# Performance work log

Measured on AMD Instinct MI355X. Metric: run time of the kernel, lower is better.

Reference implementation:

```python
import jax, jax.numpy as jnp
import numpy as np

NH = 8      # num_heads
NP_ = 4     # num_points

def setup_inputs() -> dict:
    key = jax.random.key(0)
    ks = jax.random.split(key, 12)
    B, N, C = 8, 4096, 256
    query = jax.random.normal(ks[0], (B, N, C), jnp.float32)
    value = jax.random.normal(ks[1], (B, N, C), jnp.float32)
    reference_points = jax.random.uniform(ks[2], (B, N, 2), jnp.float32)
    xav = lambda k, i, o: jax.random.normal(k, (i, o), jnp.float32) * np.sqrt(2.0 / (i + o)).astype(np.float32)
    W_off = jax.random.normal(ks[3], (C, NH * NP_ * 2), jnp.float32) * 0.02  # small offsets (orig inits to 0)
    b_off = jax.random.normal(ks[4], (NH * NP_ * 2,), jnp.float32) * 0.02
    W_attn = xav(ks[5], C, NH * NP_)
    b_attn = jnp.zeros((NH * NP_,), jnp.float32)
    W_val = xav(ks[6], C, C)
    b_val = jnp.zeros((C,), jnp.float32)
    W_out = xav(ks[7], C, C)
    b_out = jnp.zeros((C,), jnp.float32)
    return dict(query=query, value=value, reference_points=reference_points,
                W_off=W_off, b_off=b_off, W_attn=W_attn, b_attn=b_attn,
                W_val=W_val, b_val=b_val, W_out=W_out, b_out=b_out)

def _deform_attn(query, value, reference_points, W_off, b_off, W_attn, b_attn, W_val, b_val, W_out, b_out):
    B, N, C = query.shape
    HW = value.shape[1]
    H = W = int(np.sqrt(HW))  # static
    hd = C // NH
    # value projection -> [B, NH, H*W, hd]
    vals = (value @ W_val + b_val).reshape(B, H, W, NH, hd)
    vals = vals.transpose(0, 3, 1, 2, 4).reshape(B, NH, H * W, hd)
    # offsets [B,N,NH,P,2] in [-0.5,0.5]; attention weights softmax over P
    off = jnp.tanh((query @ W_off + b_off).reshape(B, N, NH, NP_, 2)) * 0.5
    attn = jax.nn.softmax((query @ W_attn + b_attn).reshape(B, N, NH, NP_), axis=-1)
    # sampling locations in [0,1], then grid coords in [-1,1] (x=width, y=height)
    loc = jnp.clip(reference_points[:, :, None, None, :] + off, 0.0, 1.0)
    g = loc * 2.0 - 1.0
    # torch grid_sample, align_corners=False: pixel = (g+1)*size/2 - 0.5
    x = (g[..., 0] + 1.0) * (W * 0.5) - 0.5
    y = (g[..., 1] + 1.0) * (H * 0.5) - 0.5
    x0f = jnp.floor(x); y0f = jnp.floor(y)
    wx1 = x - x0f; wx0 = 1.0 - wx1
    wy1 = y - y0f; wy0 = 1.0 - wy1
    x0 = x0f.astype(jnp.int32); x1 = x0 + 1
    y0 = y0f.astype(jnp.int32); y1 = y0 + 1

    def corner(xi, yi, w):  # xi,yi,w: [B,N,NH,P]; zero padding outside
        valid = (xi >= 0) & (xi < W) & (yi >= 0) & (yi < H)
        idx = jnp.clip(yi, 0, H - 1) * W + jnp.clip(xi, 0, W - 1)
        idx_h = idx.transpose(0, 2, 1, 3).reshape(B, NH, N * NP_)      # [B,NH,N*P]
        gat = jnp.take_along_axis(vals, idx_h[..., None], axis=2)      # [B,NH,N*P,hd]
        wv = jnp.where(valid, w, 0.0).transpose(0, 2, 1, 3).reshape(B, NH, N * NP_)
        return gat * wv[..., None]

    sampled = (corner(x0, y0, wx0 * wy0) + corner(x1, y0, wx1 * wy0)
               + corner(x0, y1, wx0 * wy1) + corner(x1, y1, wx1 * wy1))
    sampled = sampled.reshape(B, NH, N, NP_, hd)
    attn_h = attn.transpose(0, 2, 1, 3)                                 # [B,NH,N,P]
    out = jnp.einsum('bhnpd,bhnp->bnhd', sampled, attn_h).reshape(B, N, C)
    return out @ W_out + b_out  # dropout is identity in eval

def reference(query, value, reference_points, W_off, b_off, W_attn, b_attn, W_val, b_val, W_out, b_out):
    return _deform_attn(query, value, reference_points, W_off, b_off, W_attn, b_attn, W_val, b_val, W_out, b_out)
```

## Files before the change

### kernel.cpp

```cpp
#include <hip/hip_runtime.h>
#include <math.h>

#define NHEAD 8
#define NPT 4
#define HDIM 32
#define IMG 64
#define CDIM 256
#define NQ 4096
#define BATCH 8
#define MTOT (BATCH * NQ)

typedef __attribute__((ext_vector_type(8))) short bf16x8;
typedef __attribute__((ext_vector_type(4))) float f32x4;

__device__ __forceinline__ unsigned short f2b(float f) {
    union { float f; unsigned u; } v; v.f = f;
    unsigned r = (v.u + 0x7FFFu + ((v.u >> 16) & 1u)) >> 16;
    return (unsigned short)r;
}
__device__ __forceinline__ float b2f(unsigned short u) {
    union { unsigned u; float f; } v; v.u = ((unsigned)u) << 16;
    return v.f;
}

#define SWZ(row, col) ((col) ^ (((row) & 7) << 3))


__global__ __launch_bounds__(256)
void cvt_weights_kernel(const float* __restrict__ Wv, const float* __restrict__ Wo,
                        const float* __restrict__ Woff, const float* __restrict__ Wattn,
                        const float* __restrict__ boff, const float* __restrict__ battn,
                        unsigned short* __restrict__ Wv_t, unsigned short* __restrict__ Wo_t,
                        unsigned short* __restrict__ Wl_h, unsigned short* __restrict__ Wl_l,
                        float* __restrict__ bias_lin)
{
    int tid = blockIdx.x * 256 + threadIdx.x;
    int n = tid & 255, k = tid >> 8;
    Wv_t[n * 256 + k] = f2b(Wv[k * 256 + n]);
    Wo_t[n * 256 + k] = f2b(Wo[k * 256 + n]);
    if (tid < 128 * 256) {
        int nn = tid >> 8;
        int kk = tid & 255;
        float v = (nn < 64) ? Woff[kk * 64 + nn]
                : (nn < 96) ? Wattn[kk * 32 + (nn - 64)] : 0.f;
        unsigned short hi = f2b(v);
        unsigned short lo = f2b(v - b2f(hi));
        Wl_h[nn * 256 + kk] = hi;
        Wl_l[nn * 256 + kk] = lo;
    }
    if (tid < 128)
        bias_lin[tid] = (tid < 64) ? boff[tid] : (tid < 96) ? battn[tid - 64] : 0.f;
}

__global__ __launch_bounds__(256)
void lin_gemm_kernel(const float* __restrict__ Q,
                     const unsigned short* __restrict__ Wl_h,
                     const unsigned short* __restrict__ Wl_l,
                     const float* __restrict__ bias,
                     float* __restrict__ lin)
{
    __shared__ unsigned short Ah[128][64], Al[128][64];
    __shared__ unsigned short Bh[128][64], Bl[128][64];

    const int tid  = threadIdx.x;
    const int lane = tid & 63;
    const int wid  = tid >> 6;
    const int gm = ((blockIdx.x & 7) << 12) + ((blockIdx.x >> 3) << 7);
    const int wr = (wid >> 1) * 64;
    const int wc = (wid & 1) * 64;
    const int l15 = lane & 15;
    const int lk  = (lane >> 4) * 8;

    f32x4 acc[4][4];
    #pragma unroll
    for (int m = 0; m < 4; ++m)
        #pragma unroll
        for (int n = 0; n < 4; ++n)
            #pragma unroll
            for (int r = 0; r < 4; ++r) acc[m][n][r] = 0.f;

    for (int k0 = 0; k0 < 256; k0 += 64) {
        #pragma unroll
        for (int it = 0; it < 4; ++it) {
            const int chunk = it * 256 + tid;
            const int row = chunk >> 3;
            const int kc  = (chunk & 7) << 3;
            const float4* src = (const float4*)&Q[(size_t)(gm + row) * 256 + k0 + kc];
            const float4 a = src[0], b = src[1];
            float f[8] = {a.x, a.y, a.z, a.w, b.x, b.y, b.z, b.w};
            unsigned short h[8], l[8];
            #pragma unroll
            for (int j = 0; j < 8; ++j) {
                h[j] = f2b(f[j]);
                l[j] = f2b(f[j] - b2f(h[j]));
            }
            const int sc = SWZ(row, kc);
            *(uint4*)&Ah[row][sc] = *(const uint4*)h;
            *(uint4*)&Al[row][sc] = *(const uint4*)l;
            *(uint4*)&Bh[row][sc] = *(const uint4*)&Wl_h[(size_t)row * 256 + k0 + kc];
            *(uint4*)&Bl[row][sc] = *(const uint4*)&Wl_l[(size_t)row * 256 + k0 + kc];
        }
        __syncthreads();

        #pragma unroll
        for (int kk = 0; kk < 64; kk += 32) {
            bf16x8 ah[4], al[4];
            #pragma unroll
            for (int m = 0; m < 4; ++m) {
                const int r = wr + m * 16 + l15;
                const int c = SWZ(r, kk + lk);
                ah[m] = *(const bf16x8*)&Ah[r][c];
                al[m] = *(const bf16x8*)&Al[r][c];
            }
            if (wc == 0) {
                bf16x8 bh[4], bl[4];
                #pragma unroll
                for (int n = 0; n < 4; ++n) {
                    const int r = n * 16 + l15;
                    const int c = SWZ(r, kk + lk);
                    bh[n] = *(const bf16x8*)&Bh[r][c];
                    bl[n] = *(const bf16x8*)&Bl[r][c];
                }
                #pragma unroll
                for (int m = 0; m < 4; ++m)
                    #pragma unroll
                    for (int n = 0; n < 4; ++n) {
                        acc[m][n] = __builtin_amdgcn_mfma_f32_16x16x32_bf16(ah[m], bh[n], acc[m][n], 0, 0, 0);
                        acc[m][n] = __builtin_amdgcn_mfma_f32_16x16x32_bf16(ah[m], bl[n], acc[m][n], 0, 0, 0);
                        acc[m][n] = __builtin_amdgcn_mfma_f32_16x16x32_bf16(al[m], bh[n], acc[m][n], 0, 0, 0);
                    }
            } else {
                bf16x8 bh[2], bl[2];
                #pragma unroll
                for (int n = 0; n < 2; ++n) {
                    const int r = 64 + n * 16 + l15;
                    const int c = SWZ(r, kk + lk);
                    bh[n] = *(const bf16x8*)&Bh[r][c];
                    bl[n] = *(const bf16x8*)&Bl[r][c];
                }
                #pragma unroll
                for (int m = 0; m < 4; ++m)
                    #pragma unroll
                    for (int n = 0; n < 2; ++n) {
                        acc[m][n] = __builtin_amdgcn_mfma_f32_16x16x32_bf16(ah[m], bh[n], acc[m][n], 0, 0, 0);
                        acc[m][n] = __builtin_amdgcn_mfma_f32_16x16x32_bf16(ah[m], bl[n], acc[m][n], 0, 0, 0);
                        acc[m][n] = __builtin_amdgcn_mfma_f32_16x16x32_bf16(al[m], bh[n], acc[m][n], 0, 0, 0);
                    }
            }
        }
        __syncthreads();
    }

    const int cr = (lane >> 4) * 4;
    #pragma unroll
    for (int n = 0; n < 4; ++n) {
        const int col = wc + n * 16 + l15;
        if (col < 96) {
            const float bv = bias[col];
            #pragma unroll
            for (int m = 0; m < 4; ++m)
                #pragma unroll
                for (int r = 0; r < 4; ++r) {
                    const int row = gm + wr + m * 16 + cr + r;
                    lin[(size_t)row * 96 + col] = acc[m][n][r] + bv;
                }
        }
    }
}

template<bool A_F32, bool OUT_BF16>
__global__ __launch_bounds__(256)
void gemm_bf16_kernel(const void* __restrict__ Ap,
                      const unsigned short* __restrict__ Bt,
                      const float* __restrict__ bias,
                      void* __restrict__ C)
{
    __shared__ unsigned short As[128][64];
    __shared__ unsigned short Bs[128][64];

    const int tid  = threadIdx.x;
    const int lane = tid & 63;
    const int wid  = tid >> 6;
    const int gm = ((blockIdx.x & 7) << 12) + ((blockIdx.x >> 3) << 7);
    const int gn = blockIdx.y * 128;
    const int wr = (wid >> 1) * 64;
    const int wc = (wid & 1) * 64;
    const int l15 = lane & 15;
    const int lk  = (lane >> 4) * 8;

    f32x4 acc[4][4];
    #pragma unroll
    for (int m = 0; m < 4; ++m)
        #pragma unroll
        for (int n = 0; n < 4; ++n)
            #pragma unroll
            for (int r = 0; r < 4; ++r) acc[m][n][r] = 0.f;

    for (int k0 = 0; k0 < 256; k0 += 64) {
        #pragma unroll
        for (int it = 0; it < 4; ++it) {
            const int chunk = it * 256 + tid;
            const int row = chunk >> 3;
            const int kc  = (chunk & 7) << 3;
            const int sc = SWZ(row, kc);
            if (A_F32) {
                const float4* src = (const float4*)&((const float*)Ap)[(size_t)(gm + row) * 256 + k0 + kc];
                const float4 a = src[0], b = src[1];
                float f[8] = {a.x, a.y, a.z, a.w, b.x, b.y, b.z, b.w};
                unsigned short h[8];
                #pragma unroll
                for (int j = 0; j < 8; ++j) h[j] = f2b(f[j]);
                *(uint4*)&As[row][sc] = *(const uint4*)h;
            } else {
                *(uint4*)&As[row][sc] =
                    *(const uint4*)&((const unsigned short*)Ap)[(size_t)(gm + row) * 256 + k0 + kc];
            }
            *(uint4*)&Bs[row][sc] = *(const uint4*)&Bt[(size_t)(gn + row) * 256 + k0 + kc];
        }
        __syncthreads();

        #pragma unroll
        for (int kk = 0; kk < 64; kk += 32) {
            bf16x8 a[4], b[4];
            #pragma unroll
            for (int m = 0; m < 4; ++m) {
                const int r = wr + m * 16 + l15;
                a[m] = *(const bf16x8*)&As[r][SWZ(r, kk + lk)];
            }
            #pragma unroll
            for (int n = 0; n < 4; ++n) {
                const int r = wc + n * 16 + l15;
                b[n] = *(const bf16x8*)&Bs[r][SWZ(r, kk + lk)];
            }
            #pragma unroll
            for (int m = 0; m < 4; ++m)
                #pragma unroll
                for (int n = 0; n < 4; ++n)
                    acc[m][n] = __builtin_amdgcn_mfma_f32_16x16x32_bf16(a[m], b[n], acc[m][n], 0, 0, 0);
        }
        __syncthreads();
    }

    const int cr = (lane >> 4) * 4;
    #pragma unroll
    for (int n = 0; n < 4; ++n) {
        const int col = gn + wc + n * 16 + l15;
        const float bv = bias[col];
        #pragma unroll
        for (int m = 0; m < 4; ++m) {
            #pragma unroll
            for (int r = 0; r < 4; ++r) {
                const int row = gm + wr + m * 16 + cr + r;
                const float v = acc[m][n][r] + bv;
                if (OUT_BF16)
                    ((unsigned short*)C)[(size_t)row * 256 + col] = f2b(v);
                else
                    ((float*)C)[(size_t)row * 256 + col] = v;
            }
        }
    }
}

__global__ __launch_bounds__(256)
void sample_gather_kernel(const unsigned short* __restrict__ projv,
                          const float* __restrict__ lin,
                          const float* __restrict__ refp,
                          unsigned short* __restrict__ sampled)
{
    __shared__ float4 s_w[4][32];
    __shared__ unsigned s_xy[4][32];

    const int i = blockIdx.x;
    const int b = i & 7;
    const int bn0 = (b << 12) + ((i >> 3) << 2);
    const int t = threadIdx.x;

    if (t < 128) {
        const int sub = t >> 5;
        const int q = t & 31;
        const int h = q >> 2;
        const int p = q & 3;
        const int bn = bn0 + sub;
        const float2 rp = *(const float2*)&refp[(size_t)bn * 2];
        const float2 ol = *(const float2*)&lin[(size_t)bn * 96 + h * 8 + p * 2];
        const float al  = lin[(size_t)bn * 96 + 64 + q];

        float mx = al;
        mx = fmaxf(mx, __shfl_xor(mx, 1));
        mx = fmaxf(mx, __shfl_xor(mx, 2));
        float e = expf(al - mx);
        float s = e;
        s += __shfl_xor(s, 1);
        s += __shfl_xor(s, 2);
        const float aw = e / s;

        const float lx = fminf(fmaxf(rp.x + tanhf(ol.x) * 0.5f, 0.f), 1.f);
        const float ly = fminf(fmaxf(rp.y + tanhf(ol.y) * 0.5f, 0.f), 1.f);
        const float x = lx * (float)IMG - 0.5f;
        const float y = ly * (float)IMG - 0.5f;
        const float x0f = floorf(x), y0f = floorf(y);
        const int x0 = (int)x0f, y0 = (int)y0f;
        const float wx1 = x - x0f, wx0 = 1.f - wx1;
        const float wy1 = y - y0f, wy0 = 1.f - wy1;
        const bool vx0 = (x0 >= 0), vx1 = (x0 + 1 < IMG);
        const bool vy0 = (y0 >= 0), vy1 = (y0 + 1 < IMG);
        float4 w;
        w.x = (vx0 && vy0) ? wx0 * wy0 * aw : 0.f;
        w.y = (vx1 && vy0) ? wx1 * wy0 * aw : 0.f;
        w.z = (vx0 && vy1) ? wx0 * wy1 * aw : 0.f;
        w.w = (vx1 && vy1) ? wx1 * wy1 * aw : 0.f;
        const int x0c = min(max(x0, 0), IMG - 1), x1c = min(max(x0 + 1, 0), IMG - 1);
        const int y0c = min(max(y0, 0), IMG - 1), y1c = min(max(y0 + 1, 0), IMG - 1);
        s_w[sub][q] = w;
        s_xy[sub][q] = (unsigned)x0c | ((unsigned)x1c << 8) | ((unsigned)y0c << 16) | ((unsigned)y1c << 24);
    }
    __syncthreads();

    const int sub = t >> 6;
    const int l = t & 63;
    const int h2 = l >> 3;
    const int cp = l & 7;
    const int bn = bn0 + sub;
    const unsigned short* vbase = projv + ((size_t)b << 20) + h2 * HDIM + cp * 4;

    float a0 = 0.f, a1 = 0.f, a2 = 0.f, a3 = 0.f;
    #pragma unroll
    for (int p = 0; p < 4; ++p) {
        const float4 w = s_w[sub][h2 * 4 + p];
        const unsigned xy = s_xy[sub][h2 * 4 + p];
        const int x0 = xy & 255, x1 = (xy >> 8) & 255;
        const int y0 = (xy >> 16) & 255, y1 = xy >> 24;
        const uint2 u00 = *(const uint2*)&vbase[(((y0 << 6) + x0) << 8)];
        const uint2 u01 = *(const uint2*)&vbase[(((y0 << 6) + x1) << 8)];
        const uint2 u10 = *(const uint2*)&vbase[(((y1 << 6) + x0) << 8)];
        const uint2 u11 = *(const uint2*)&vbase[(((y1 << 6) + x1) << 8)];
        a0 += w.x * b2f((unsigned short)(u00.x & 0xffff)) + w.y * b2f((unsigned short)(u01.x & 0xffff))
            + w.z * b2f((unsigned short)(u10.x & 0xffff)) + w.w * b2f((unsigned short)(u11.x & 0xffff));
        a1 += w.x * b2f((unsigned short)(u00.x >> 16)) + w.y * b2f((unsigned short)(u01.x >> 16))
            + w.z * b2f((unsigned short)(u10.x >> 16)) + w.w * b2f((unsigned short)(u11.x >> 16));
        a2 += w.x * b2f((unsigned short)(u00.y & 0xffff)) + w.y * b2f((unsigned short)(u01.y & 0xffff))
            + w.z * b2f((unsigned short)(u10.y & 0xffff)) + w.w * b2f((unsigned short)(u11.y & 0xffff));
        a3 += w.x * b2f((unsigned short)(u00.y >> 16)) + w.y * b2f((unsigned short)(u01.y >> 16))
            + w.z * b2f((unsigned short)(u10.y >> 16)) + w.w * b2f((unsigned short)(u11.y >> 16));
    }
    uint2 outp;
    outp.x = (unsigned)f2b(a0) | ((unsigned)f2b(a1) << 16);
    outp.y = (unsigned)f2b(a2) | ((unsigned)f2b(a3) << 16);
    *(uint2*)&sampled[(size_t)bn * 256 + h2 * HDIM + cp * 4] = outp;
}

extern "C" void kernel_launch(void* const* d_in, const int* in_sizes, int n_in,
                              void* d_out, int out_size, void* d_ws, size_t ws_size,
                              hipStream_t stream)
{
    const float* query  = (const float*)d_in[0];
    const float* value  = (const float*)d_in[1];
    const float* refp   = (const float*)d_in[2];
    const float* W_off  = (const float*)d_in[3];
    const float* b_off  = (const float*)d_in[4];
    const float* W_attn = (const float*)d_in[5];
    const float* b_attn = (const float*)d_in[6];
    const float* W_val  = (const float*)d_in[7];
    const float* b_val  = (const float*)d_in[8];
    const float* W_out  = (const float*)d_in[9];
    const float* b_out  = (const float*)d_in[10];
    float* out = (float*)d_out;

    char* ws = (char*)d_ws;
    unsigned short* projv    = (unsigned short*)ws; ws += (size_t)MTOT * 256 * 2;
    unsigned short* sampled  = (unsigned short*)ws; ws += (size_t)MTOT * 256 * 2;
    float*          lin      = (float*)ws;          ws += (size_t)MTOT * 96 * 4;
    unsigned short* Wv_t     = (unsigned short*)ws; ws += 256 * 256 * 2;
    unsigned short* Wo_t     = (unsigned short*)ws; ws += 256 * 256 * 2;
    unsigned short* Wl_h     = (unsigned short*)ws; ws += 128 * 256 * 2;
    unsigned short* Wl_l     = (unsigned short*)ws; ws += 128 * 256 * 2;
    float*          bias_lin = (float*)ws;          ws += 128 * 4;

    dim3 blk(256);

    cvt_weights_kernel<<<dim3(256), blk, 0, stream>>>(W_val, W_out, W_off, W_attn, b_off, b_attn,
                                                      Wv_t, Wo_t, Wl_h, Wl_l, bias_lin);

    gemm_bf16_kernel<true, true><<<dim3(MTOT / 128, 2), blk, 0, stream>>>(value, Wv_t, b_val, projv);

    lin_gemm_kernel<<<dim3(MTOT / 128), blk, 0, stream>>>(query, Wl_h, Wl_l, bias_lin, lin);

    sample_gather_kernel<<<dim3(MTOT / 4), blk, 0, stream>>>(projv, lin, refp, sampled);

    gemm_bf16_kernel<false, false><<<dim3(MTOT / 128, 2), blk, 0, stream>>>(sampled, Wo_t, b_out, out);
}
```

Baseline: 72.04 us.

## Use direct global-to-LDS loads for bf16 GEMM tiles and double queries per gather block

Weight and bf16 activation tiles in the GEMM kernels are now loaded with global_load_lds (direct-to-LDS, 16 bytes per lane), with the XOR swizzle applied on the global source column, so the data no longer passes through registers. The sampling kernel now handles 8 queries per block in two passes, with all 256 threads computing sampling metadata, which halves the grid size. The goal is to cut register traffic and instruction count in the tile loads and to amortize block setup in the gather. In exchange it depends on direct-to-LDS layout semantics being correct and gives the gather kernel less block-level parallelism.

```diff
diff --git a/kernel.cpp b/kernel.cpp
--- a/kernel.cpp
+++ b/kernel.cpp
@@ -24,6 +24,12 @@
 }
 
 #define SWZ(row, col) ((col) ^ (((row) & 7) << 3))
+
+__device__ __forceinline__ void gload16(const void* src, void* ldsbase) {
+    __builtin_amdgcn_global_load_lds(
+        (const __attribute__((address_space(1))) void*)src,
+        (__attribute__((address_space(3))) void*)ldsbase, 16, 0, 0);
+}
 
 
 __global__ __launch_bounds__(256)
@@ -70,6 +76,8 @@
     const int wc = (wid & 1) * 64;
     const int l15 = lane & 15;
     const int lk  = (lane >> 4) * 8;
+    const int rl  = lane >> 3;
+    const int ch  = (lane & 7) ^ (rl & 7);
 
     f32x4 acc[4][4];
     #pragma unroll
@@ -80,6 +88,12 @@
             for (int r = 0; r < 4; ++r) acc[m][n][r] = 0.f;
 
     for (int k0 = 0; k0 < 256; k0 += 64) {
+        #pragma unroll
+        for (int it = 0; it < 4; ++it) {
+            const int br = it * 32 + wid * 8;
+            gload16(&Wl_h[(size_t)(br + rl) * 256 + k0 + ch * 8], &Bh[br][0]);
+            gload16(&Wl_l[(size_t)(br + rl) * 256 + k0 + ch * 8], &Bl[br][0]);
+        }
         #pragma unroll
         for (int it = 0; it < 4; ++it) {
             const int chunk = it * 256 + tid;
@@ -97,8 +111,6 @@
             const int sc = SWZ(row, kc);
             *(uint4*)&Ah[row][sc] = *(const uint4*)h;
             *(uint4*)&Al[row][sc] = *(const uint4*)l;
-            *(uint4*)&Bh[row][sc] = *(const uint4*)&Wl_h[(size_t)row * 256 + k0 + kc];
-            *(uint4*)&Bl[row][sc] = *(const uint4*)&Wl_l[(size_t)row * 256 + k0 + kc];
         }
         __syncthreads();
 
@@ -187,6 +199,8 @@
     const int wc = (wid & 1) * 64;
     const int l15 = lane & 15;
     const int lk  = (lane >> 4) * 8;
+    const int rl  = lane >> 3;
+    const int ch  = (lane & 7) ^ (rl & 7);
 
     f32x4 acc[4][4];
     #pragma unroll
@@ -199,23 +213,29 @@
     for (int k0 = 0; k0 < 256; k0 += 64) {
         #pragma unroll
         for (int it = 0; it < 4; ++it) {
-            const int chunk = it * 256 + tid;
-            const int row = chunk >> 3;
-            const int kc  = (chunk & 7) << 3;
-            const int sc = SWZ(row, kc);
-            if (A_F32) {
+            const int br = it * 32 + wid * 8;
+            gload16(&Bt[(size_t)(gn + br + rl) * 256 + k0 + ch * 8], &Bs[br][0]);
+        }
+        if (A_F32) {
+            #pragma unroll
+            for (int it = 0; it < 4; ++it) {
+                const int chunk = it * 256 + tid;
+                const int row = chunk >> 3;
+                const int kc  = (chunk & 7) << 3;
                 const float4* src = (const float4*)&((const float*)Ap)[(size_t)(gm + row) * 256 + k0 + kc];
                 const float4 a = src[0], b = src[1];
                 float f[8] = {a.x, a.y, a.z, a.w, b.x, b.y, b.z, b.w};
                 unsigned short h[8];
                 #pragma unroll
                 for (int j = 0; j < 8; ++j) h[j] = f2b(f[j]);
-                *(uint4*)&As[row][sc] = *(const uint4*)h;
-            } else {
-                *(uint4*)&As[row][sc] =
-                    *(const uint4*)&((const unsigned short*)Ap)[(size_t)(gm + row) * 256 + k0 + kc];
-            }
-            *(uint4*)&Bs[row][sc] = *(const uint4*)&Bt[(size_t)(gn + row) * 256 + k0 + kc];
+                *(uint4*)&As[row][SWZ(row, kc)] = *(const uint4*)h;
+            }
+        } else {
+            #pragma unroll
+            for (int it = 0; it < 4; ++it) {
+                const int br = it * 32 + wid * 8;
+                gload16(&((const unsigned short*)Ap)[(size_t)(gm + br + rl) * 256 + k0 + ch * 8], &As[br][0]);
+            }
         }
         __syncthreads();
 
@@ -267,15 +287,15 @@
                           const float* __restrict__ refp,
                           unsigned short* __restrict__ sampled)
 {
-    __shared__ float4 s_w[4][32];
-    __shared__ unsigned s_xy[4][32];
+    __shared__ float4 s_w[8][32];
+    __shared__ unsigned s_xy[8][32];
 
     const int i = blockIdx.x;
     const int b = i & 7;
-    const int bn0 = (b << 12) + ((i >> 3) << 2);
+    const int bn0 = (b << 12) + ((i >> 3) << 3);
     const int t = threadIdx.x;
 
-    if (t < 128) {
+    {
         const int sub = t >> 5;
         const int q = t & 31;
         const int h = q >> 2;
@@ -316,37 +336,41 @@
     }
     __syncthreads();
 
-    const int sub = t >> 6;
     const int l = t & 63;
     const int h2 = l >> 3;
     const int cp = l & 7;
-    const int bn = bn0 + sub;
     const unsigned short* vbase = projv + ((size_t)b << 20) + h2 * HDIM + cp * 4;
 
-    float a0 = 0.f, a1 = 0.f, a2 = 0.f, a3 = 0.f;
     #pragma unroll
-    for (int p = 0; p < 4; ++p) {
-        const float4 w = s_w[sub][h2 * 4 + p];
-        const unsigned xy = s_xy[sub][h2 * 4 + p];
-        const int x0 = xy & 255, x1 = (xy >> 8) & 255;
-        const int y0 = (xy >> 16) & 255, y1 = xy >> 24;
-        const uint2 u00 = *(const uint2*)&vbase[(((y0 << 6) + x0) << 8)];
-        const uint2 u01 = *(const uint2*)&vbase[(((y0 << 6) + x1) << 8)];
-        const uint2 u10 = *(const uint2*)&vbase[(((y1 << 6) + x0) << 8)];
-        const uint2 u11 = *(const uint2*)&vbase[(((y1 << 6) + x1) << 8)];
-        a0 += w.x * b2f((unsigned short)(u00.x & 0xffff)) + w.y * b2f((unsigned short)(u01.x & 0xffff))
-            + w.z * b2f((unsigned short)(u10.x & 0xffff)) + w.w * b2f((unsigned short)(u11.x & 0xffff));
-        a1 += w.x * b2f((unsigned short)(u00.x >> 16)) + w.y * b2f((unsigned short)(u01.x >> 16))
-            + w.z * b2f((unsigned short)(u10.x >> 16)) + w.w * b2f((unsigned short)(u11.x >> 16));
-        a2 += w.x * b2f((unsigned short)(u00.y & 0xffff)) + w.y * b2f((unsigned short)(u01.y & 0xffff))
-            + w.z * b2f((unsigned short)(u10.y & 0xffff)) + w.w * b2f((unsigned short)(u11.y & 0xffff));
-        a3 += w.x * b2f((unsigned short)(u00.y >> 16)) + w.y * b2f((unsigned short)(u01.y >> 16))
-            + w.z * b2f((unsigned short)(u10.y >> 16)) + w.w * b2f((unsigned short)(u11.y >> 16));
-    }
-    uint2 outp;
-    outp.x = (unsigned)f2b(a0) | ((unsigned)f2b(a1) << 16);
-    outp.y = (unsigned)f2b(a2) | ((unsigned)f2b(a3) << 16);
-    *(uint2*)&sampled[(size_t)bn * 256 + h2 * HDIM + cp * 4] = outp;
+    for (int pass = 0; pass < 2; ++pass) {
+        const int sub = (t >> 6) + pass * 4;
+        const int bn = bn0 + sub;
+
+        float a0 = 0.f, a1 = 0.f, a2 = 0.f, a3 = 0.f;
+        #pragma unroll
+        for (int p = 0; p < 4; ++p) {
+            const float4 w = s_w[sub][h2 * 4 + p];
+            const unsigned xy = s_xy[sub][h2 * 4 + p];
+            const int x0 = xy & 255, x1 = (xy >> 8) & 255;
+            const int y0 = (xy >> 16) & 255, y1 = xy >> 24;
+            const uint2 u00 = *(const uint2*)&vbase[(((y0 << 6) + x0) << 8)];
+            const uint2 u01 = *(const uint2*)&vbase[(((y0 << 6) + x1) << 8)];
+            const uint2 u10 = *(const uint2*)&vbase[(((y1 << 6) + x0) << 8)];
+            const uint2 u11 = *(const uint2*)&vbase[(((y1 << 6) + x1) << 8)];
+            a0 += w.x * b2f((unsigned short)(u00.x & 0xffff)) + w.y * b2f((unsigned short)(u01.x & 0xffff))
+                + w.z * b2f((unsigned short)(u10.x & 0xffff)) + w.w * b2f((unsigned short)(u11.x & 0xffff));
+            a1 += w.x * b2f((unsigned short)(u00.x >> 16)) + w.y * b2f((unsigned short)(u01.x >> 16))
+                + w.z * b2f((unsigned short)(u10.x >> 16)) + w.w * b2f((unsigned short)(u11.x >> 16));
+            a2 += w.x * b2f((unsigned short)(u00.y & 0xffff)) + w.y * b2f((unsigned short)(u01.y & 0xffff))
+                + w.z * b2f((unsigned short)(u10.y & 0xffff)) + w.w * b2f((unsigned short)(u11.y & 0xffff));
+            a3 += w.x * b2f((unsigned short)(u00.y >> 16)) + w.y * b2f((unsigned short)(u01.y >> 16))
+                + w.z * b2f((unsigned short)(u10.y >> 16)) + w.w * b2f((unsigned short)(u11.y >> 16));
+        }
+        uint2 outp;
+        outp.x = (unsigned)f2b(a0) | ((unsigned)f2b(a1) << 16);
+        outp.y = (unsigned)f2b(a2) | ((unsigned)f2b(a3) << 16);
+        *(uint2*)&sampled[(size_t)bn * 256 + h2 * HDIM + cp * 4] = outp;
+    }
 }
 
 extern "C" void kernel_launch(void* const* d_in, const int* in_sizes, int n_in,
@@ -385,7 +409,7 @@
 
     lin_gemm_kernel<<<dim3(MTOT / 128), blk, 0, stream>>>(query, Wl_h, Wl_l, bias_lin, lin);
 
-    sample_gather_kernel<<<dim3(MTOT / 4), blk, 0, stream>>>(projv, lin, refp, sampled);
+    sample_gather_kernel<<<dim3(MTOT / 8), blk, 0, stream>>>(projv, lin, refp, sampled);
 
     gemm_bf16_kernel<false, false><<<dim3(MTOT / 128, 2), blk, 0, stream>>>(sampled, Wo_t, b_out, out);
 }
```

Measured after the change: 73.93 us. 2.6% more time.
